# Kernel optimization log

Measured on AMD Instinct MI355X. Metric: run time of the kernel, lower is better.

Reference implementation:

```python
import jax, jax.numpy as jnp
import numpy as np

N_NODES = 50000
N_EDGES = 1600000
D = 64
L = 4
ALPHA = 0.1


def setup_inputs() -> dict:
    key = jax.random.key(0)
    ks = jax.random.split(key, 6)
    x = jax.random.normal(ks[0], (N_NODES, D), dtype=jnp.float32)
    w = jax.random.uniform(ks[1], (N_EDGES,), dtype=jnp.float32)
    # linear layer params, scaled ~ 1/sqrt(fan_in)
    W = jax.random.normal(ks[2], (L, D, D), dtype=jnp.float32) * (1.0 / np.sqrt(D))
    b = jnp.zeros((L, D), dtype=jnp.float32)
    # GPR temp schedule: alpha*(1-alpha)^k, last = (1-alpha)^L
    temp = ALPHA * (1.0 - ALPHA) ** np.arange(L + 1)
    temp[-1] = (1.0 - ALPHA) ** L
    temp = jnp.asarray(temp, dtype=jnp.float32)
    src = jax.random.randint(ks[3], (N_EDGES,), 0, N_NODES, dtype=jnp.int32)
    dst = jax.random.randint(ks[4], (N_EDGES,), 0, N_NODES, dtype=jnp.int32)
    return {"x": x, "w": w, "W": W, "b": b, "temp": temp, "src": src, "dst": dst}


def reference(x, w, W, b, temp, src, dst):
    # Eval mode: dropout / dropout_adj are identity; edge_attn=False.
    n = x.shape[0]
    hidden = x * temp[0]
    num_layers = W.shape[0]
    for i in range(num_layers):
        # linear: h = x @ W_i^T + b_i
        h = jnp.einsum('nd,od->no', x, W[i]) + b[i]
        # u_mul_e + sum: gather src features, scale by edge weight, scatter-sum to dst
        m = h[src] * w[:, None]                       # [E, D]
        x = jax.ops.segment_sum(m, dst, num_segments=n)  # [N, D]
        x = jax.nn.relu(x)
        hidden = hidden + x * temp[i + 1]
    return hidden
```

## Files before the change

### kernel.cpp

```cpp
#include <hip/hip_runtime.h>
#include <hip/hip_fp16.h>

#define NN 50000
#define NE 1600000
#define DD 64
#define NBK 782
#define TILE 4096
#define NTB 391
#define SCAP 3072

typedef _Float16 half8 __attribute__((ext_vector_type(8)));
typedef float float4v __attribute__((ext_vector_type(4)));

__global__ __launch_bounds__(256) void wswz_kernel(const float* __restrict__ W,
                                                   _Float16* __restrict__ Wswz,
                                                   int* __restrict__ gcur) {
    int flat = blockIdx.x * 256 + threadIdx.x;
    if (blockIdx.x == 0) {
        for (int k = threadIdx.x; k < NBK; k += 256) gcur[k] = 0;
    }
    int l = flat >> 12, r = flat & 4095;
    int j = r & 7, lane = (r >> 3) & 63, kt = (r >> 9) & 1, nt = r >> 10;
    int n = nt * 16 + (lane & 15);
    int k = kt * 32 + ((lane >> 4) * 8) + j;
    Wswz[flat] = (_Float16)W[l * 4096 + n * 64 + k];
}

__global__ __launch_bounds__(256) void fill_kernel(const int* __restrict__ src,
                                                   const int* __restrict__ dst,
                                                   const float* __restrict__ w,
                                                   int* __restrict__ gcur,
                                                   unsigned int* __restrict__ tmp) {
    __shared__ unsigned int data[TILE];
    __shared__ unsigned short bktl[TILE];
    __shared__ int cnt[NBK], bas[NBK], rnk[NBK];
    __shared__ int sc[1024];
    int t = threadIdx.x;
    for (int k = t; k < NBK; k += 256) { cnt[k] = 0; rnk[k] = 0; }
    __syncthreads();
    int base = blockIdx.x * TILE;
    unsigned int er_e[TILE / 256];
    int er_b[TILE / 256];
#pragma unroll
    for (int k = 0; k < TILE / 256; ++k) {
        int i = base + k * 256 + t;
        if (i < NE) {
            int d = dst[i];
            unsigned int wq = (unsigned int)(w[i] * 1024.0f);
            if (wq > 1023u) wq = 1023u;
            er_e[k] = (unsigned int)src[i] | ((unsigned int)(d & 63) << 16) | (wq << 22);
            er_b[k] = d >> 6;
            atomicAdd(&cnt[er_b[k]], 1);
        }
    }
    __syncthreads();
    for (int k = t; k < NBK; k += 256) {
        int c = cnt[k];
        bas[k] = c ? atomicAdd(&gcur[k], c) : 0;
    }
    for (int k = t; k < 1024; k += 256) sc[k] = (k < NBK) ? cnt[k] : 0;
    __syncthreads();
    for (int s = 1; s < 1024; s <<= 1) {
        int v0[4];
#pragma unroll
        for (int j = 0; j < 4; ++j) {
            int idx = t + j * 256;
            v0[j] = (idx >= s) ? sc[idx - s] : 0;
        }
        __syncthreads();
#pragma unroll
        for (int j = 0; j < 4; ++j) sc[t + j * 256] += v0[j];
        __syncthreads();
    }
#pragma unroll
    for (int k = 0; k < TILE / 256; ++k) {
        int i = base + k * 256 + t;
        if (i < NE) {
            int b = er_b[k];
            int r = atomicAdd(&rnk[b], 1);
            int pos = (sc[b] - cnt[b]) + r;
            data[pos] = er_e[k];
            bktl[pos] = (unsigned short)b;
        }
    }
    __syncthreads();
    int tot = NE - base; if (tot > TILE) tot = TILE;
    for (int idx = t; idx < tot; idx += 256) {
        int b = bktl[idx];
        int lb = sc[b] - cnt[b];
        tmp[(size_t)b * SCAP + bas[b] + (idx - lb)] = data[idx];
    }
}

__global__ __launch_bounds__(256) void sortgemm_kernel(const unsigned int* __restrict__ tmp,
                                                       const int* __restrict__ gcur,
                                                       unsigned int* __restrict__ csr,
                                                       int2* __restrict__ off2,
                                                       const float* __restrict__ x32,
                                                       const _Float16* __restrict__ Wg,
                                                       const float* __restrict__ bl,
                                                       _Float16* __restrict__ h) {
    __shared__ unsigned int sdata[SCAP];
    __shared__ int cnt[64], nb[64], pos[64];
    int b = blockIdx.x, t = threadIdx.x;

    int wave = t >> 6, lane = t & 63;
    int m = lane & 15, q = lane >> 4;
    int node0 = b * 64 + wave * 16;
    int arow = node0 + m; if (arow >= NN) arow = NN - 1;
    const float4* xr = (const float4*)(x32 + (size_t)arow * 64);
    float4 f0 = xr[2 * q], f1 = xr[2 * q + 1];
    float4 f2 = xr[8 + 2 * q], f3 = xr[8 + 2 * q + 1];

    int beg = b * SCAP, n = gcur[b];
    if (t < 64) cnt[t] = 0;
    __syncthreads();
    for (int i = t; i < n; i += 256) {
        unsigned int e = tmp[beg + i];
        sdata[i] = e;
        atomicAdd(&cnt[(e >> 16) & 63u], 1);
    }
    __syncthreads();
    if (t == 0) {
        int a = 0;
        for (int k = 0; k < 64; ++k) { nb[k] = a; pos[k] = a; a += cnt[k]; }
    }
    __syncthreads();
    for (int i = t; i < n; i += 256) {
        unsigned int e = sdata[i];
        int d = (int)((e >> 16) & 63u);
        float wf = ((float)(e >> 22) + 0.5f) * (1.0f / 1024.0f);
        unsigned int wh = (unsigned int)__half_as_ushort(__float2half_rn(wf));
        int r = atomicAdd(&pos[d], 1);
        csr[beg + r] = (e & 0xffffu) | (wh << 16);
    }
    if (t < 64) {
        int node = b * 64 + t;
        if (node < NN) {
            int2 oe;
            oe.x = beg + nb[t];
            oe.y = beg + nb[t] + cnt[t];
            off2[node] = oe;
        }
    }

    half8 a0, a1;
    a0[0] = (_Float16)f0.x; a0[1] = (_Float16)f0.y; a0[2] = (_Float16)f0.z; a0[3] = (_Float16)f0.w;
    a0[4] = (_Float16)f1.x; a0[5] = (_Float16)f1.y; a0[6] = (_Float16)f1.z; a0[7] = (_Float16)f1.w;
    a1[0] = (_Float16)f2.x; a1[1] = (_Float16)f2.y; a1[2] = (_Float16)f2.z; a1[3] = (_Float16)f2.w;
    a1[4] = (_Float16)f3.x; a1[5] = (_Float16)f3.y; a1[6] = (_Float16)f3.z; a1[7] = (_Float16)f3.w;
    const half8* Wf = (const half8*)Wg;
    float4v acc[4];
#pragma unroll
    for (int nt = 0; nt < 4; ++nt) acc[nt] = (float4v){0.f, 0.f, 0.f, 0.f};
#pragma unroll
    for (int nt = 0; nt < 4; ++nt) {
        half8 b0 = Wf[(nt * 2 + 0) * 64 + lane];
        half8 b1 = Wf[(nt * 2 + 1) * 64 + lane];
        acc[nt] = __builtin_amdgcn_mfma_f32_16x16x32_f16(a0, b0, acc[nt], 0, 0, 0);
        acc[nt] = __builtin_amdgcn_mfma_f32_16x16x32_f16(a1, b1, acc[nt], 0, 0, 0);
    }
#pragma unroll
    for (int nt = 0; nt < 4; ++nt) {
        float bv = bl[nt * 16 + m];
#pragma unroll
        for (int r = 0; r < 4; ++r) {
            int node = node0 + q * 4 + r;
            if (node < NN)
                h[(size_t)node * 64 + nt * 16 + m] = (_Float16)(acc[nt][r] + bv);
        }
    }
}

__global__ __launch_bounds__(256) void pull_fused(const uint4* __restrict__ h16,
                                                  const unsigned int* __restrict__ csr,
                                                  const int2* __restrict__ off2,
                                                  float4* __restrict__ out,
                                                  const float4* __restrict__ x32,
                                                  const float* __restrict__ temp,
                                                  const _Float16* __restrict__ Wg,
                                                  const float* __restrict__ bl,
                                                  _Float16* __restrict__ hout,
                                                  int layer) {
    __shared__ _Float16 vsh[16 * 72];
    int t = threadIdx.x;
    int lane = t & 63;
    int slot = lane >> 4, g = (lane >> 3) & 1, sub = lane & 7;
    int node0 = blockIdx.x * 16;
    int nloc = (t >> 6) * 4 + slot;
    int node = node0 + nloc;
    bool tail = (node0 + 16 > NN);
    if (tail) {
        for (int k = t; k < 16 * 72; k += 256) vsh[k] = (_Float16)0.f;
        __syncthreads();
    }

    int nclamp = node < NN ? node : NN - 1;
    int2 oe = off2[nclamp];
    int deg = (node < NN) ? (oe.y - oe.x) : 0;
    int beg = oe.x;
    int dmax = deg;
    dmax = max(dmax, __shfl_xor(dmax, 16));
    dmax = max(dmax, __shfl_xor(dmax, 32));
    int sl = lane & 15;
    float acc[8];
#pragma unroll
    for (int k = 0; k < 8; ++k) acc[k] = 0.f;

    int chunks = (dmax + 15) >> 4;
    unsigned int e = (sl < deg) ? csr[beg + sl] : 0u;
    for (int c = 0; c < chunks; ++c) {
        int nidx = ((c + 1) << 4) + sl;
        unsigned int enext = (nidx < deg) ? csr[beg + nidx] : 0u;
#pragma unroll
        for (int j = 0; j < 8; ++j) {
            unsigned int ej = (unsigned int)__shfl((int)e, (slot << 4) + j * 2 + g);
            int s = (int)(ej & 0xffffu);
            __half wh = __ushort_as_half((unsigned short)(ej >> 16));
            uint4 hv = h16[(size_t)s * 8 + sub];
            const __half* hp = (const __half*)&hv;
            float wf = (float)wh;
#pragma unroll
            for (int k = 0; k < 8; ++k)
                acc[k] += (float)hp[k] * wf;
        }
        e = enext;
    }
#pragma unroll
    for (int k = 0; k < 8; ++k) acc[k] += __shfl_xor(acc[k], 8);

    if (g == 0 && node < NN) {
        float tk = temp[layer + 1];
        float v[8];
#pragma unroll
        for (int k = 0; k < 8; ++k) v[k] = fmaxf(acc[k], 0.f);
        __half2 p[4];
#pragma unroll
        for (int k = 0; k < 4; ++k) p[k] = __floats2half2_rn(v[2 * k], v[2 * k + 1]);
        *(uint4*)&vsh[nloc * 72 + sub * 8] = *(const uint4*)p;
        int gi = node * 16 + sub * 2;
        float4 o0, o1;
        if (layer == 0) {
            float t0 = temp[0];
            float4 a = x32[gi], bq = x32[gi + 1];
            o0.x = a.x * t0;  o0.y = a.y * t0;  o0.z = a.z * t0;  o0.w = a.w * t0;
            o1.x = bq.x * t0; o1.y = bq.y * t0; o1.z = bq.z * t0; o1.w = bq.w * t0;
        } else {
            o0 = out[gi]; o1 = out[gi + 1];
        }
        o0.x += v[0] * tk; o0.y += v[1] * tk; o0.z += v[2] * tk; o0.w += v[3] * tk;
        o1.x += v[4] * tk; o1.y += v[5] * tk; o1.z += v[6] * tk; o1.w += v[7] * tk;
        out[gi]     = o0;
        out[gi + 1] = o1;
    }

    if (Wg != nullptr) {
        __syncthreads();
        int wave = t >> 6;
        int m = lane & 15, q = lane >> 4;
        half8 a0 = *(const half8*)&vsh[m * 72 + q * 8];
        half8 a1 = *(const half8*)&vsh[m * 72 + 32 + q * 8];
        const half8* Wf = (const half8*)Wg;
        half8 b0 = Wf[(wave * 2 + 0) * 64 + lane];
        half8 b1 = Wf[(wave * 2 + 1) * 64 + lane];
        float4v d = (float4v){0.f, 0.f, 0.f, 0.f};
        d = __builtin_amdgcn_mfma_f32_16x16x32_f16(a0, b0, d, 0, 0, 0);
        d = __builtin_amdgcn_mfma_f32_16x16x32_f16(a1, b1, d, 0, 0, 0);
        float bv = bl[wave * 16 + m];
#pragma unroll
        for (int r = 0; r < 4; ++r) {
            int n2 = node0 + q * 4 + r;
            if (n2 < NN)
                hout[(size_t)n2 * 64 + wave * 16 + m] = (_Float16)(d[r] + bv);
        }
    }
}

extern "C" void kernel_launch(void* const* d_in, const int* in_sizes, int n_in,
                              void* d_out, int out_size, void* d_ws, size_t ws_size,
                              hipStream_t stream) {
    const float* x    = (const float*)d_in[0];
    const float* w    = (const float*)d_in[1];
    const float* W    = (const float*)d_in[2];
    const float* b    = (const float*)d_in[3];
    const float* temp = (const float*)d_in[4];
    const int*   src  = (const int*)d_in[5];
    const int*   dst  = (const int*)d_in[6];
    float* out = (float*)d_out;

    _Float16*     hA   = (_Float16*)d_ws;
    _Float16*     hB   = hA + (size_t)NN * DD;
    unsigned int* csr  = (unsigned int*)(hB + (size_t)NN * DD);
    unsigned int* tmp  = csr + (size_t)NBK * SCAP;
    int*          gcur = (int*)(tmp + (size_t)NBK * SCAP);
    int2*         off2 = (int2*)(gcur + NBK);
    _Float16*     Wswz = (_Float16*)(off2 + NN);

    wswz_kernel<<<64, 256, 0, stream>>>(W, Wswz, gcur);
    fill_kernel<<<NTB, 256, 0, stream>>>(src, dst, w, gcur, tmp);
    sortgemm_kernel<<<NBK, 256, 0, stream>>>(tmp, gcur, csr, off2, x, Wswz, b, hA);

    const int PG = (NN + 15) / 16;
    _Float16* hin  = hA;
    _Float16* hout = hB;
    for (int l = 0; l < 4; ++l) {
        const _Float16* Wn = (l < 3) ? (Wswz + (size_t)(l + 1) * 4096) : nullptr;
        const float*    bn = (l < 3) ? (b + (size_t)(l + 1) * DD) : nullptr;
        pull_fused<<<PG, 256, 0, stream>>>(
            (const uint4*)hin, csr, off2, (float4*)out, (const float4*)x,
            temp, Wn, bn, hout, l);
        _Float16* sw = hin; hin = hout; hout = sw;
    }
}
```

Baseline: 226.3 us.

## Double-buffer neighbor gathers in aggregation and vectorize edge loads in fill

```diff
diff --git a/kernel.cpp b/kernel.cpp
--- a/kernel.cpp
+++ b/kernel.cpp
@@ -42,15 +42,39 @@
     unsigned int er_e[TILE / 256];
     int er_b[TILE / 256];
 #pragma unroll
-    for (int k = 0; k < TILE / 256; ++k) {
-        int i = base + k * 256 + t;
-        if (i < NE) {
-            int d = dst[i];
-            unsigned int wq = (unsigned int)(w[i] * 1024.0f);
-            if (wq > 1023u) wq = 1023u;
-            er_e[k] = (unsigned int)src[i] | ((unsigned int)(d & 63) << 16) | (wq << 22);
-            er_b[k] = d >> 6;
-            atomicAdd(&cnt[er_b[k]], 1);
+    for (int kk = 0; kk < 4; ++kk) {
+        int i0 = base + kk * 1024 + t * 4;
+        if (i0 + 3 < NE) {
+            int4   d4 = *(const int4*)(dst + i0);
+            int4   s4 = *(const int4*)(src + i0);
+            float4 w4 = *(const float4*)(w + i0);
+            const int*   dp = (const int*)&d4;
+            const int*   sp = (const int*)&s4;
+            const float* wp = (const float*)&w4;
+#pragma unroll
+            for (int u = 0; u < 4; ++u) {
+                int d = dp[u];
+                unsigned int wq = (unsigned int)(wp[u] * 1024.0f);
+                if (wq > 1023u) wq = 1023u;
+                er_e[kk * 4 + u] = (unsigned int)sp[u] | ((unsigned int)(d & 63) << 16) | (wq << 22);
+                er_b[kk * 4 + u] = d >> 6;
+                atomicAdd(&cnt[d >> 6], 1);
+            }
+        } else {
+#pragma unroll
+            for (int u = 0; u < 4; ++u) {
+                int i = i0 + u;
+                if (i < NE) {
+                    int d = dst[i];
+                    unsigned int wq = (unsigned int)(w[i] * 1024.0f);
+                    if (wq > 1023u) wq = 1023u;
+                    er_e[kk * 4 + u] = (unsigned int)src[i] | ((unsigned int)(d & 63) << 16) | (wq << 22);
+                    er_b[kk * 4 + u] = d >> 6;
+                    atomicAdd(&cnt[d >> 6], 1);
+                } else {
+                    er_b[kk * 4 + u] = -1;
+                }
+            }
         }
     }
     __syncthreads();
@@ -74,8 +98,7 @@
     }
 #pragma unroll
     for (int k = 0; k < TILE / 256; ++k) {
-        int i = base + k * 256 + t;
-        if (i < NE) {
+        if (er_b[k] >= 0) {
             int b = er_b[k];
             int r = atomicAdd(&rnk[b], 1);
             int pos = (sc[b] - cnt[b]) + r;
@@ -199,33 +222,50 @@
     int2 oe = off2[nclamp];
     int deg = (node < NN) ? (oe.y - oe.x) : 0;
     int beg = oe.x;
-    int dmax = deg;
-    dmax = max(dmax, __shfl_xor(dmax, 16));
-    dmax = max(dmax, __shfl_xor(dmax, 32));
     int sl = lane & 15;
     float acc[8];
 #pragma unroll
     for (int k = 0; k < 8; ++k) acc[k] = 0.f;
 
-    int chunks = (dmax + 15) >> 4;
-    unsigned int e = (sl < deg) ? csr[beg + sl] : 0u;
-    for (int c = 0; c < chunks; ++c) {
-        int nidx = ((c + 1) << 4) + sl;
-        unsigned int enext = (nidx < deg) ? csr[beg + nidx] : 0u;
-#pragma unroll
-        for (int j = 0; j < 8; ++j) {
-            unsigned int ej = (unsigned int)__shfl((int)e, (slot << 4) + j * 2 + g);
-            int s = (int)(ej & 0xffffu);
-            __half wh = __ushort_as_half((unsigned short)(ej >> 16));
-            uint4 hv = h16[(size_t)s * 8 + sub];
-            const __half* hp = (const __half*)&hv;
-            float wf = (float)wh;
-#pragma unroll
-            for (int k = 0; k < 8; ++k)
-                acc[k] += (float)hp[k] * wf;
-        }
-        e = enext;
-    }
+#define GB(EV, HV, WF)                                                        \
+    _Pragma("unroll")                                                         \
+    for (int j = 0; j < 8; ++j) {                                             \
+        unsigned int ej = (unsigned int)__shfl((int)(EV), (slot << 4) + j * 2 + g); \
+        WF[j] = (float)__ushort_as_half((unsigned short)(ej >> 16));          \
+        HV[j] = h16[(size_t)(ej & 0xffffu) * 8 + sub];                        \
+    }
+#define FB(HV, WF)                                                            \
+    _Pragma("unroll")                                                         \
+    for (int j = 0; j < 8; ++j) {                                             \
+        const __half* hp = (const __half*)&HV[j];                             \
+        _Pragma("unroll")                                                     \
+        for (int k = 0; k < 8; ++k) acc[k] += (float)hp[k] * WF[j];           \
+    }
+
+    int chunks = (deg + 15) >> 4;
+    uint4 hvA[8], hvB[8];
+    float wfA[8], wfB[8];
+    if (chunks > 0) {
+        unsigned int eA = (sl < deg) ? csr[beg + sl] : 0u;
+        GB(eA, hvA, wfA);
+        for (int c = 0; c < chunks; ) {
+            int ni = ((c + 1) << 4) + sl;
+            unsigned int eB = (ni < deg) ? csr[beg + ni] : 0u;
+            bool hasB = (c + 1) < chunks;
+            if (hasB) { GB(eB, hvB, wfB); }
+            FB(hvA, wfA);
+            ++c; if (!hasB) break;
+            int ni2 = ((c + 1) << 4) + sl;
+            unsigned int eA2 = (ni2 < deg) ? csr[beg + ni2] : 0u;
+            bool hasA = (c + 1) < chunks;
+            if (hasA) { GB(eA2, hvA, wfA); }
+            FB(hvB, wfB);
+            ++c; if (!hasA) break;
+        }
+    }
+#undef GB
+#undef FB
+
 #pragma unroll
     for (int k = 0; k < 8; ++k) acc[k] += __shfl_xor(acc[k], 8);
 
```

Result: slower. 270.9 us (+19.7%).
